# Kernel tuning notes

Hardware: AMD Instinct MI355X
Metric: run time of the kernel (lower is better)

The kernel has to match this reference:

```python
import jax, jax.numpy as jnp
import numpy as np

DIM = 2048
K = 4

def setup_inputs() -> dict:
    key = jax.random.key(0)
    k1, k2, k3 = jax.random.split(key, 3)
    x = jax.random.normal(k1, (4, 4096, DIM), dtype=jnp.float32)
    # torch Conv1d(dim, dim, K, groups=dim): weight [D,1,K] -> store as [D,K]; bias [D]
    bound = 1.0 / np.sqrt(K)  # fan_in = (in_channels/groups)*K = K
    w = jax.random.uniform(k2, (DIM, K), dtype=jnp.float32, minval=-bound, maxval=bound)
    b = jax.random.uniform(k3, (DIM,), dtype=jnp.float32, minval=-bound, maxval=bound)
    return {"x": x, "w": w, "b": b}

def reference(x, w, b):
    # Causal depthwise conv1d on [B,S,D]: out[t,d] = b[d] + sum_k w[d,k]*x[t+k-(K-1),d]
    B, S, D = x.shape
    xp = jnp.pad(x, ((0, 0), (K - 1, 0), (0, 0)))  # left-pad time axis
    y = b  # broadcasts over [B,S,D]
    for k in range(K):  # small fixed kernel loop (K=4)
        y = y + xp[:, k:k + S, :] * w[:, k]
    return y
```

## Files before the change

### kernel.cpp

```cpp
#include <hip/hip_runtime.h>

#define DIM    2048
#define SEQ    4096
#define BATCH  4
#define KW     4
#define TCHUNK 16

typedef float fvec4 __attribute__((ext_vector_type(4)));

__global__ __launch_bounds__(256) void ShortConv1D_78855599554935_kernel(
    const float* __restrict__ x, const float* __restrict__ w,
    const float* __restrict__ bias, float* __restrict__ out)
{
    constexpr int D4 = DIM / 4;
    constexpr int NT = SEQ / TCHUNK;

    int idx  = blockIdx.x * blockDim.x + threadIdx.x;
    int d4   = idx & (D4 - 1);
    int rest = idx >> 9;
    int tc   = rest & (NT - 1);
    int bb   = rest >> 8;

    const fvec4* __restrict__ x4 = (const fvec4*)x;
    const fvec4* __restrict__ w4 = (const fvec4*)w;
    const fvec4* __restrict__ b4 = (const fvec4*)bias;
    fvec4* __restrict__ o4 = (fvec4*)out;

    long base = ((long)bb * SEQ + (long)tc * TCHUNK) * D4 + d4;

    fvec4 w0 = w4[d4 * 4 + 0];
    fvec4 w1 = w4[d4 * 4 + 1];
    fvec4 w2 = w4[d4 * 4 + 2];
    fvec4 w3 = w4[d4 * 4 + 3];
    fvec4 bv = b4[d4];

    fvec4 xv[TCHUNK + 3];
    if (tc > 0) {
        xv[0] = x4[base - 3 * D4];
        xv[1] = x4[base - 2 * D4];
        xv[2] = x4[base - 1 * D4];
    } else {
        xv[0] = (fvec4)(0.f);
        xv[1] = (fvec4)(0.f);
        xv[2] = (fvec4)(0.f);
    }
#pragma unroll
    for (int t = 0; t < TCHUNK; ++t) {
        xv[3 + t] = x4[base + t * D4];
    }

    __builtin_amdgcn_sched_barrier(0);

#pragma unroll
    for (int t = 0; t < TCHUNK; ++t) {
        fvec4 a  = xv[t];
        fvec4 bq = xv[t + 1];
        fvec4 c  = xv[t + 2];
        fvec4 dd = xv[t + 3];
        fvec4 r;
        r.x = bv.x + w0.x * a.x + w0.y * bq.x + w0.z * c.x + w0.w * dd.x;
        r.y = bv.y + w1.x * a.y + w1.y * bq.y + w1.z * c.y + w1.w * dd.y;
        r.z = bv.z + w2.x * a.z + w2.y * bq.z + w2.z * c.z + w2.w * dd.z;
        r.w = bv.w + w3.x * a.w + w3.y * bq.w + w3.z * c.w + w3.w * dd.w;
        __builtin_nontemporal_store(r, &o4[base + t * D4]);
    }
}

extern "C" void kernel_launch(void* const* d_in, const int* in_sizes, int n_in,
                              void* d_out, int out_size, void* d_ws, size_t ws_size,
                              hipStream_t stream) {
    const float* x = (const float*)d_in[0];
    const float* w = (const float*)d_in[1];
    const float* b = (const float*)d_in[2];
    float* out = (float*)d_out;

    constexpr int D4 = DIM / 4;
    constexpr int NT = SEQ / TCHUNK;
    int total_threads = BATCH * NT * D4;
    int block = 256;
    int grid = total_threads / block;

    ShortConv1D_78855599554935_kernel<<<grid, block, 0, stream>>>(x, w, b, out);
}
```

Before: 236.6 us.

## Use persistent grid looping over batches with double-buffered chunk loads

Result: no change. 238.4 us (+0.8%).

```diff
diff --git a/kernel.cpp b/kernel.cpp
--- a/kernel.cpp
+++ b/kernel.cpp
@@ -4,29 +4,30 @@
 #define SEQ    4096
 #define BATCH  4
 #define KW     4
-#define TCHUNK 16
+#define TCHUNK 8
 
 typedef float fvec4 __attribute__((ext_vector_type(4)));
 
-__global__ __launch_bounds__(256) void ShortConv1D_78855599554935_kernel(
+constexpr int D4       = DIM / 4;
+constexpr int NT       = SEQ / TCHUNK;
+constexpr int NCHUNK   = BATCH * NT * D4;
+constexpr int NBLOCK   = 1024;
+constexpr int BLOCKSZ  = 256;
+constexpr int NTHREADS = NBLOCK * BLOCKSZ;
+constexpr int ITERS    = NCHUNK / NTHREADS;
+
+__global__ __launch_bounds__(BLOCKSZ, 4) void ShortConv1D_78855599554935_kernel(
     const float* __restrict__ x, const float* __restrict__ w,
     const float* __restrict__ bias, float* __restrict__ out)
 {
-    constexpr int D4 = DIM / 4;
-    constexpr int NT = SEQ / TCHUNK;
-
-    int idx  = blockIdx.x * blockDim.x + threadIdx.x;
-    int d4   = idx & (D4 - 1);
-    int rest = idx >> 9;
-    int tc   = rest & (NT - 1);
-    int bb   = rest >> 8;
+    int idx = blockIdx.x * BLOCKSZ + threadIdx.x;
+    int d4  = idx & (D4 - 1);
+    int tc  = (idx >> 9) & (NT - 1);
 
     const fvec4* __restrict__ x4 = (const fvec4*)x;
     const fvec4* __restrict__ w4 = (const fvec4*)w;
     const fvec4* __restrict__ b4 = (const fvec4*)bias;
     fvec4* __restrict__ o4 = (fvec4*)out;
-
-    long base = ((long)bb * SEQ + (long)tc * TCHUNK) * D4 + d4;
 
     fvec4 w0 = w4[d4 * 4 + 0];
     fvec4 w1 = w4[d4 * 4 + 1];
@@ -34,36 +35,62 @@
     fvec4 w3 = w4[d4 * 4 + 3];
     fvec4 bv = b4[d4];
 
-    fvec4 xv[TCHUNK + 3];
-    if (tc > 0) {
-        xv[0] = x4[base - 3 * D4];
-        xv[1] = x4[base - 2 * D4];
-        xv[2] = x4[base - 1 * D4];
-    } else {
-        xv[0] = (fvec4)(0.f);
-        xv[1] = (fvec4)(0.f);
-        xv[2] = (fvec4)(0.f);
-    }
-#pragma unroll
-    for (int t = 0; t < TCHUNK; ++t) {
-        xv[3 + t] = x4[base + t * D4];
-    }
+    long base0 = (long)tc * TCHUNK * D4 + (long)d4;
+    constexpr long BSTRIDE = (long)SEQ * D4;
 
+    fvec4 xa[TCHUNK + 3], xb[TCHUNK + 3];
+
+#define LOADCH(xv, base)                                                    \
+    do {                                                                    \
+        if (tc > 0) {                     \
+            xv[0] = x4[(base) - 3 * D4];                                    \
+            xv[1] = x4[(base) - 2 * D4];                                    \
+            xv[2] = x4[(base) - 1 * D4];                                    \
+        } else {                                                            \
+            xv[0] = (fvec4)(0.f);                                           \
+            xv[1] = (fvec4)(0.f);                                           \
+            xv[2] = (fvec4)(0.f);                                           \
+        }                                                                   \
+        _Pragma("unroll")                                                   \
+        for (int t = 0; t < TCHUNK; ++t) xv[3 + t] = x4[(base) + t * D4];   \
+    } while (0)
+
+#define STORECH(xv, base)                                                   \
+    do {                                                                    \
+        _Pragma("unroll")                                                   \
+        for (int t = 0; t < TCHUNK; ++t) {                                  \
+            fvec4 a  = xv[t];                                               \
+            fvec4 bq = xv[t + 1];                                           \
+            fvec4 cc = xv[t + 2];                                           \
+            fvec4 dd = xv[t + 3];                                           \
+            fvec4 r;                                                        \
+            r.x = bv.x + w0.x * a.x + w0.y * bq.x + w0.z * cc.x + w0.w * dd.x; \
+            r.y = bv.y + w1.x * a.y + w1.y * bq.y + w1.z * cc.y + w1.w * dd.y; \
+            r.z = bv.z + w2.x * a.z + w2.y * bq.z + w2.z * cc.z + w2.w * dd.z; \
+            r.w = bv.w + w3.x * a.w + w3.y * bq.w + w3.z * cc.w + w3.w * dd.w; \
+            __builtin_nontemporal_store(r, &o4[(base) + t * D4]);           \
+        }                                                                   \
+    } while (0)
+
+    LOADCH(xa, base0);
     __builtin_amdgcn_sched_barrier(0);
 
 #pragma unroll
-    for (int t = 0; t < TCHUNK; ++t) {
-        fvec4 a  = xv[t];
-        fvec4 bq = xv[t + 1];
-        fvec4 c  = xv[t + 2];
-        fvec4 dd = xv[t + 3];
-        fvec4 r;
-        r.x = bv.x + w0.x * a.x + w0.y * bq.x + w0.z * c.x + w0.w * dd.x;
-        r.y = bv.y + w1.x * a.y + w1.y * bq.y + w1.z * c.y + w1.w * dd.y;
-        r.z = bv.z + w2.x * a.z + w2.y * bq.z + w2.z * c.z + w2.w * dd.z;
-        r.w = bv.w + w3.x * a.w + w3.y * bq.w + w3.z * c.w + w3.w * dd.w;
-        __builtin_nontemporal_store(r, &o4[base + t * D4]);
+    for (int it = 0; it < ITERS; it += 2) {
+        long baseB = base0 + (long)(it + 1) * BSTRIDE;
+        LOADCH(xb, baseB);
+        __builtin_amdgcn_sched_barrier(0);
+        STORECH(xa, base0 + (long)it * BSTRIDE);
+
+        if (it + 2 < ITERS) {
+            LOADCH(xa, base0 + (long)(it + 2) * BSTRIDE);
+            __builtin_amdgcn_sched_barrier(0);
+        }
+        STORECH(xb, baseB);
     }
+
+#undef LOADCH
+#undef STORECH
 }
 
 extern "C" void kernel_launch(void* const* d_in, const int* in_sizes, int n_in,
@@ -74,11 +101,5 @@
     const float* b = (const float*)d_in[2];
     float* out = (float*)d_out;
 
-    constexpr int D4 = DIM / 4;
-    constexpr int NT = SEQ / TCHUNK;
-    int total_threads = BATCH * NT * D4;
-    int block = 256;
-    int grid = total_threads / block;
-
-    ShortConv1D_78855599554935_kernel<<<grid, block, 0, stream>>>(x, w, b, out);
+    ShortConv1D_78855599554935_kernel<<<NBLOCK, BLOCKSZ, 0, stream>>>(x, w, b, out);
 }
```
